# Performance work log

Hardware: AMD Instinct MI355X
Metric: run time of the kernel (lower is better)

## Reference

```python
import jax, jax.numpy as jnp
import numpy as np

B, L, C = 64, 4096, 16
PL, PC, NP, D, FS = 128, 8, 64, 64, 100  # patch_size_L, patch_size_C, num_patches, output_dim, f_s


def setup_inputs() -> dict:
    key = jax.random.key(0)
    ks = jax.random.split(key, 9)
    x = jax.random.normal(ks[0], (B, L, C), dtype=jnp.float32)
    start_L = jax.random.randint(ks[1], (B, NP), 0, L - PL + 1, dtype=jnp.int32)
    idx_C = jax.random.randint(ks[2], (B, NP, PC), 0, C, dtype=jnp.int32)
    W1 = jax.random.normal(ks[3], (2 * PC + 1, D), dtype=jnp.float32) * 0.2
    b1 = jax.random.normal(ks[4], (D,), dtype=jnp.float32) * 0.02
    W2 = jax.random.normal(ks[5], (2 * D + 1, D), dtype=jnp.float32) * 0.1
    b2 = jax.random.normal(ks[6], (D,), dtype=jnp.float32) * 0.02
    W3 = jax.random.normal(ks[7], (PL * D, D), dtype=jnp.float32) * 0.01
    b3 = jax.random.normal(ks[8], (D,), dtype=jnp.float32) * 0.02
    return dict(x=x, start_L=start_L, idx_C=idx_C, W1=W1, b1=b1, W2=W2, b2=b2, W3=W3, b3=b3)


def reference(x, start_L, idx_C, W1, b1, W2, b2, W3, b3):
    T = 1.0 / FS
    # contiguous window indices along L (wrapped), [B, NP, PL]
    idx_L = (start_L[:, :, None] + jnp.arange(PL, dtype=jnp.int32)) % L
    # fused double gather: avoid materializing the [B, NP, L, C] broadcast of the original
    bidx = jnp.arange(B)[:, None, None, None]
    patches = x[bidx, idx_L[:, :, :, None], idx_C[:, :, None, :]]        # [B, NP, PL, PC]
    # time embedding: t = arange(L)*T gathered by idx_L
    t_patches = (idx_L.astype(jnp.float32) * T)[..., None]               # [B, NP, PL, 1]
    # channel embedding: c = arange(C) gathered by idx_C
    c_patches = jnp.broadcast_to(idx_C.astype(jnp.float32)[:, :, None, :], (B, NP, PL, PC))
    feats = jnp.concatenate([patches, t_patches, c_patches], axis=-1)    # [B, NP, PL, 2*PC+1]
    h = jax.nn.silu(feats @ W1 + b1)                                     # [B, NP, PL, D]
    # --- fft branch (computed then discarded by the original module; kept for fidelity) ---
    f = jnp.linspace(0.0, FS / 2.0, PL // 2 + 1)
    fft = jnp.fft.rfft(h, axis=-2, norm='ortho')                         # [B, NP, PL//2+1, D]
    f_patches = jnp.broadcast_to(f[None, None, :, None], (B, NP, PL // 2 + 1, 1))
    fcat = jnp.concatenate([fft.real, fft.imag, f_patches], axis=-1)     # [B, NP, PL//2+1, 2D+1]
    _unused = jax.nn.silu(fcat @ W2 + b2)
    # --- mixer on flattened patches ---
    flat = h.reshape(B, NP, PL * D)                                      # [B, NP, PL*D]
    out = jax.nn.silu(flat @ W3 + b3)                                    # [B, NP, D]
    return out
```

## Files before the change

### kernel.cpp

```cpp
#include <hip/hip_runtime.h>
#include <hip/hip_bf16.h>

#define BB 64
#define LL 4096
#define CC 16
#define PL 128
#define PC 8
#define NPP 64
#define DD 64
#define TSTEP 0.01f

#define KSPLIT 4
#define LT_PER (PL / KSPLIT)
#define NT_MAIN 256
#define NMB BB

#define FRAG_U32 (PL * 8 * 256)
#define SPLIT_STRIDE (NMB * 2 * 2 * 64 * 16)
#define PART_FLT (KSPLIT * SPLIT_STRIDE)

typedef float f32x4  __attribute__((ext_vector_type(4)));
typedef float f32x16 __attribute__((ext_vector_type(16)));
typedef int   i32x4  __attribute__((ext_vector_type(4)));
typedef short s16x8  __attribute__((ext_vector_type(8)));
typedef unsigned int u32;

__device__ __forceinline__ float silu_f(float z) {
    return z * __builtin_amdgcn_rcpf(1.0f + __expf(-z));
}
__device__ __forceinline__ u32 pk(float lo, float hi) {
    __hip_bfloat162 p = __float22bfloat162_rn(float2{lo, hi});
    u32 r;
    __builtin_memcpy(&r, &p, 4);
    return r;
}
__device__ __forceinline__ s16x8 as8(i32x4 v) {
    s16x8 r;
    __builtin_memcpy(&r, &v, 16);
    return r;
}
__device__ __forceinline__ void plswap(u32& a, u32& b) {
    auto r = __builtin_amdgcn_permlane32_swap(a, b, false, false);
    u32 tmp[2];
    __builtin_memcpy(tmp, &r, 8);
    a = tmp[0]; b = tmp[1];
}

__global__ __launch_bounds__(256) void w3_prep(const float* __restrict__ W3,
                                               u32* __restrict__ wsf) {
    const int tid  = blockIdx.x * 256 + threadIdx.x;
    const int lane = tid & 63;
    const int m    = tid >> 6;
    const int ns   = m & 1;
    const int ksub = (m >> 1) & 1;
    const int kk   = (m >> 2) & 1;
    const int ltg  = m >> 3;
    const int k0   = ltg * 64 + kk * 32 + ksub * 16 + ((lane >> 5) << 3);
    const int col  = (ns << 5) + (lane & 31);
    u32 q[4];
    #pragma unroll
    for (int jj = 0; jj < 4; ++jj)
        q[jj] = pk(W3[(size_t)(k0 + 2 * jj)     * DD + col],
                   W3[(size_t)(k0 + 2 * jj + 1) * DD + col]);
    i32x4 v; v.x = (int)q[0]; v.y = (int)q[1]; v.z = (int)q[2]; v.w = (int)q[3];
    *(i32x4*)(wsf + (size_t)m * 256 + (lane << 2)) = v;
}

__global__ __launch_bounds__(NT_MAIN) void htfe_main(
    const float* __restrict__ x, const int* __restrict__ start_L,
    const int* __restrict__ idx_C, const float* __restrict__ W1,
    const float* __restrict__ b1, const u32* __restrict__ wsf,
    float* __restrict__ part)
{
    __shared__ __align__(64) float arena[512 * 17];
    __shared__ __align__(16) u32   xq[LT_PER * 256];
    __shared__ __align__(16) u32   cq[256];
    __shared__ int sStart[64];

    const int t    = threadIdx.x;
    const int lane = t & 63;
    const int w    = t >> 6;
    const int kk   = w >> 1;
    const int ph   = w & 1;
    const int l31  = lane & 31;
    const bool loH = lane < 32;

    const int mb    = blockIdx.x & (NMB - 1);
    const int split = blockIdx.x >> 6;
    const int b     = mb;
    const int lt0   = split * LT_PER;

    if (t < 64) sStart[t] = start_L[b * NPP + t];
    const int pGat = t & 63;
    const i32x4 ciA = *(const i32x4*)(idx_C + (size_t)b * NPP * PC + pGat * 8);
    const i32x4 ciB = *(const i32x4*)(idx_C + (size_t)b * NPP * PC + pGat * 8 + 4);
    if (t < 64) {
        cq[t * 4 + 0] = pk((float)ciA.x, (float)ciA.y);
        cq[t * 4 + 1] = pk((float)ciA.z, (float)ciA.w);
        cq[t * 4 + 2] = pk((float)ciB.x, (float)ciB.y);
        cq[t * 4 + 3] = pk((float)ciB.z, (float)ciB.w);
    }
    __syncthreads();

    #pragma unroll
    for (int pass = 0; pass < 4; ++pass) {
        #pragma unroll
        for (int q = 0; q < 8; ++q) {
            const int i    = q * 256 + t;
            const int row  = i >> 2;
            const int quad = i & 3;
            const int pp   = row & 63;
            const int gRow = sStart[pp] + lt0 + pass * 8 + (row >> 6);
            const f32x4 v = *(const f32x4*)(x + ((size_t)b * LL + (size_t)gRow) * CC + quad * 4);
            *(f32x4*)(arena + row * 17 + quad * 4) = v;
        }
        __syncthreads();
        #pragma unroll
        for (int g = 0; g < 2; ++g) {
            const int rr = g * 256 + t;
            const float* rb = arena + rr * 17;
            int cis[8];
            cis[0]=ciA.x; cis[1]=ciA.y; cis[2]=ciA.z; cis[3]=ciA.w;
            cis[4]=ciB.x; cis[5]=ciB.y; cis[6]=ciB.z; cis[7]=ciB.w;
            u32 qh[4];
            #pragma unroll
            for (int c2 = 0; c2 < 4; ++c2)
                qh[c2] = pk(rb[cis[2 * c2]], rb[cis[2 * c2 + 1]]);
            u32* dst = xq + (pass * 8 + (rr >> 6)) * 256 + (rr & 63) * 4;
            i32x4 vh; vh.x=(int)qh[0]; vh.y=(int)qh[1]; vh.z=(int)qh[2]; vh.w=(int)qh[3];
            *(i32x4*)dst = vh;
        }
        __syncthreads();
    }

    const int p  = ph * 32 + l31;
    const int dA = kk * 32 + l31;
    const float startPf = (float)sStart[p];

    i32x4 a1f0;
    if (loH) {
        a1f0.x = (int)pk(W1[0 * DD + dA], W1[1 * DD + dA]);
        a1f0.y = (int)pk(W1[2 * DD + dA], W1[3 * DD + dA]);
        a1f0.z = (int)pk(W1[4 * DD + dA], W1[5 * DD + dA]);
        a1f0.w = (int)pk(W1[6 * DD + dA], W1[7 * DD + dA]);
    } else {
        a1f0.x = (int)pk(W1[ 9 * DD + dA], W1[10 * DD + dA]);
        a1f0.y = (int)pk(W1[11 * DD + dA], W1[12 * DD + dA]);
        a1f0.z = (int)pk(W1[13 * DD + dA], W1[14 * DD + dA]);
        a1f0.w = (int)pk(W1[15 * DD + dA], W1[16 * DD + dA]);
    }
    f32x16 cb16, wt16;
    #pragma unroll
    for (int r = 0; r < 16; ++r) {
        const int dr = kk * 32 + (r & 3) + 8 * (r >> 2) + 4 * (lane >> 5);
        wt16[r] = W1[8 * DD + dr];
        cb16[r] = b1[dr];
    }

    f32x16 acc0 = {}, acc1 = {};
    const u32* bsrc = wsf + ((size_t)lt0 * 8 + (size_t)kk * 4) * 256 + (lane << 2);
    const u32* xrd     = loH ? (xq + p * 4) : (cq + p * 4);
    const int  xstride = loH ? 256 : 0;

    #pragma unroll 2
    for (int lt = 0; lt < LT_PER; ++lt) {
        const i32x4 bf00 = *(const i32x4*)(bsrc);
        const i32x4 bf01 = *(const i32x4*)(bsrc + 256);
        const i32x4 bf10 = *(const i32x4*)(bsrc + 512);
        const i32x4 bf11 = *(const i32x4*)(bsrc + 768);
        bsrc += 2048;

        const i32x4 rd = *(const i32x4*)xrd;
        xrd += xstride;

        const float tf = (startPf + (float)(lt0 + lt)) * TSTEP;
        f32x16 hp;
        #pragma unroll
        for (int r = 0; r < 16; ++r) hp[r] = cb16[r] + tf * wt16[r];
        hp = __builtin_amdgcn_mfma_f32_32x32x16_bf16(as8(a1f0), as8(rd), hp, 0, 0, 0);

        u32 P[8];
        #pragma unroll
        for (int j = 0; j < 8; ++j)
            P[j] = pk(silu_f(hp[2 * j]), silu_f(hp[2 * j + 1]));

        plswap(P[0], P[2]); plswap(P[1], P[3]);
        plswap(P[4], P[6]); plswap(P[5], P[7]);
        i32x4 af0; af0.x=(int)P[0]; af0.y=(int)P[1]; af0.z=(int)P[2]; af0.w=(int)P[3];
        i32x4 af1; af1.x=(int)P[4]; af1.y=(int)P[5]; af1.z=(int)P[6]; af1.w=(int)P[7];

        acc0 = __builtin_amdgcn_mfma_f32_32x32x16_bf16(as8(af0), as8(bf00), acc0, 0, 0, 0);
        acc0 = __builtin_amdgcn_mfma_f32_32x32x16_bf16(as8(af1), as8(bf10), acc0, 0, 0, 0);
        acc1 = __builtin_amdgcn_mfma_f32_32x32x16_bf16(as8(af0), as8(bf01), acc1, 0, 0, 0);
        acc1 = __builtin_amdgcn_mfma_f32_32x32x16_bf16(as8(af1), as8(bf11), acc1, 0, 0, 0);
    }

    f32x16* redacc = (f32x16*)arena;
    __syncthreads();
    if (kk == 1) {
        redacc[(ph * 2 + 0) * 64 + lane] = acc0;
        redacc[(ph * 2 + 1) * 64 + lane] = acc1;
    }
    __syncthreads();
    if (kk == 0) {
        const f32x16 r0 = redacc[(ph * 2 + 0) * 64 + lane];
        const f32x16 r1 = redacc[(ph * 2 + 1) * 64 + lane];
        float* pd0 = part + ((((size_t)split * NMB + mb) * 2 + ph) * 2 + 0) * 1024 + (lane << 4);
        float* pd1 = pd0 + 1024;
        #pragma unroll
        for (int q = 0; q < 4; ++q) {
            f32x4 o0, o1;
            #pragma unroll
            for (int j = 0; j < 4; ++j) {
                o0[j] = acc0[q * 4 + j] + r0[q * 4 + j];
                o1[j] = acc1[q * 4 + j] + r1[q * 4 + j];
            }
            *(f32x4*)(pd0 + q * 4) = o0;
            *(f32x4*)(pd1 + q * 4) = o1;
        }
    }
}

__global__ __launch_bounds__(256) void finish_reduce(const float* __restrict__ part,
                                                     const float* __restrict__ b3,
                                                     float* __restrict__ out) {
    const int bid   = blockIdx.x;
    const int mb    = bid & 63;
    const int chunk = bid >> 6;
    const int idx10 = chunk * 256 + threadIdx.x;
    const int rq   = idx10 & 3;
    const int lane = (idx10 >> 2) & 63;
    const int ns   = (idx10 >> 8) & 1;
    const int ph   = (idx10 >> 9) & 1;
    const int l31  = lane & 31;
    const float* src = part + (((size_t)mb * 2 + ph) * 2 + ns) * 1024 + (lane << 4) + (rq << 2);
    f32x4 s = {0.f, 0.f, 0.f, 0.f};
    #pragma unroll
    for (int sp = 0; sp < KSPLIT; ++sp) {
        const f32x4 v = *(const f32x4*)(src + (size_t)sp * SPLIT_STRIDE);
        s.x += v.x; s.y += v.y; s.z += v.z; s.w += v.w;
    }
    const int col  = (ns << 5) + l31;
    const float bias = b3[col];
    #pragma unroll
    for (int j = 0; j < 4; ++j) {
        const int prow = ph * 32 + j + 8 * rq + 4 * (lane >> 5);
        out[(size_t)(mb * NPP + prow) * DD + col] = silu_f(s[j] + bias);
    }
}

extern "C" void kernel_launch(void* const* d_in, const int* in_sizes, int n_in,
                              void* d_out, int out_size, void* d_ws, size_t ws_size,
                              hipStream_t stream) {
    const float* x       = (const float*)d_in[0];
    const int*   start_L = (const int*)  d_in[1];
    const int*   idx_C   = (const int*)  d_in[2];
    const float* W1      = (const float*)d_in[3];
    const float* b1      = (const float*)d_in[4];
    const float* W3      = (const float*)d_in[7];
    const float* b3      = (const float*)d_in[8];
    float* out  = (float*)d_out;
    u32*   wsf  = (u32*)d_ws;
    float* part = (float*)(wsf + FRAG_U32);

    w3_prep<<<256, 256, 0, stream>>>(W3, wsf);
    htfe_main<<<NMB * KSPLIT, NT_MAIN, 0, stream>>>(x, start_L, idx_C, W1, b1, wsf, part);
    finish_reduce<<<256, 256, 0, stream>>>(part, b3, out);
}
```

Before: 32.19 us.

## Overlap x-row gather with MFMA compute via register-prefetched chunks

The up-front four-pass staging of gathered x rows into LDS becomes a chunked software pipeline. Each chunk's global loads are prefetched into registers while the previous chunk's MFMA loop runs, then written to LDS and gathered into bf16 fragments between chunks. This hides global-load latency behind tensor-core work instead of paying for all passes before compute starts. The cost is 32 extra VGPRs held across the compute loop, which may reduce occupancy, and the synchronisation points now sit inside the main loop.

```diff
diff --git a/kernel.cpp b/kernel.cpp
--- a/kernel.cpp
+++ b/kernel.cpp
@@ -12,6 +12,7 @@
 
 #define KSPLIT 4
 #define LT_PER (PL / KSPLIT)
+#define NCHUNK 4
 #define NT_MAIN 256
 #define NMB BB
 
@@ -102,19 +103,31 @@
     }
     __syncthreads();
 
-    #pragma unroll
-    for (int pass = 0; pass < 4; ++pass) {
+    f32x4 rv[8];
+    const int rowi  = t >> 2;
+    const int quadi = t & 3;
+
+    auto LOADROWS = [&](int c) {
         #pragma unroll
         for (int q = 0; q < 8; ++q) {
             const int i    = q * 256 + t;
             const int row  = i >> 2;
             const int quad = i & 3;
             const int pp   = row & 63;
-            const int gRow = sStart[pp] + lt0 + pass * 8 + (row >> 6);
-            const f32x4 v = *(const f32x4*)(x + ((size_t)b * LL + (size_t)gRow) * CC + quad * 4);
-            *(f32x4*)(arena + row * 17 + quad * 4) = v;
-        }
-        __syncthreads();
+            const int gRow = sStart[pp] + lt0 + c * 8 + (row >> 6);
+            rv[q] = *(const f32x4*)(x + ((size_t)b * LL + (size_t)gRow) * CC + quad * 4);
+        }
+    };
+    auto WRITEROWS = [&]() {
+        #pragma unroll
+        for (int q = 0; q < 8; ++q) {
+            const int i    = q * 256 + t;
+            const int row  = i >> 2;
+            const int quad = i & 3;
+            *(f32x4*)(arena + row * 17 + quad * 4) = rv[q];
+        }
+    };
+    auto GATHER = [&](int c) {
         #pragma unroll
         for (int g = 0; g < 2; ++g) {
             const int rr = g * 256 + t;
@@ -126,12 +139,19 @@
             #pragma unroll
             for (int c2 = 0; c2 < 4; ++c2)
                 qh[c2] = pk(rb[cis[2 * c2]], rb[cis[2 * c2 + 1]]);
-            u32* dst = xq + (pass * 8 + (rr >> 6)) * 256 + (rr & 63) * 4;
+            u32* dst = xq + (c * 8 + (rr >> 6)) * 256 + (rr & 63) * 4;
             i32x4 vh; vh.x=(int)qh[0]; vh.y=(int)qh[1]; vh.z=(int)qh[2]; vh.w=(int)qh[3];
             *(i32x4*)dst = vh;
         }
-        __syncthreads();
-    }
+    };
+    (void)rowi; (void)quadi;
+
+    LOADROWS(0);
+    WRITEROWS();
+    __syncthreads();
+    GATHER(0);
+    LOADROWS(1);
+    __syncthreads();
 
     const int p  = ph * 32 + l31;
     const int dA = kk * 32 + l31;
@@ -162,37 +182,46 @@
     const u32* xrd     = loH ? (xq + p * 4) : (cq + p * 4);
     const int  xstride = loH ? 256 : 0;
 
-    #pragma unroll 2
-    for (int lt = 0; lt < LT_PER; ++lt) {
-        const i32x4 bf00 = *(const i32x4*)(bsrc);
-        const i32x4 bf01 = *(const i32x4*)(bsrc + 256);
-        const i32x4 bf10 = *(const i32x4*)(bsrc + 512);
-        const i32x4 bf11 = *(const i32x4*)(bsrc + 768);
-        bsrc += 2048;
-
-        const i32x4 rd = *(const i32x4*)xrd;
-        xrd += xstride;
-
-        const float tf = (startPf + (float)(lt0 + lt)) * TSTEP;
-        f32x16 hp;
-        #pragma unroll
-        for (int r = 0; r < 16; ++r) hp[r] = cb16[r] + tf * wt16[r];
-        hp = __builtin_amdgcn_mfma_f32_32x32x16_bf16(as8(a1f0), as8(rd), hp, 0, 0, 0);
-
-        u32 P[8];
-        #pragma unroll
-        for (int j = 0; j < 8; ++j)
-            P[j] = pk(silu_f(hp[2 * j]), silu_f(hp[2 * j + 1]));
-
-        plswap(P[0], P[2]); plswap(P[1], P[3]);
-        plswap(P[4], P[6]); plswap(P[5], P[7]);
-        i32x4 af0; af0.x=(int)P[0]; af0.y=(int)P[1]; af0.z=(int)P[2]; af0.w=(int)P[3];
-        i32x4 af1; af1.x=(int)P[4]; af1.y=(int)P[5]; af1.z=(int)P[6]; af1.w=(int)P[7];
-
-        acc0 = __builtin_amdgcn_mfma_f32_32x32x16_bf16(as8(af0), as8(bf00), acc0, 0, 0, 0);
-        acc0 = __builtin_amdgcn_mfma_f32_32x32x16_bf16(as8(af1), as8(bf10), acc0, 0, 0, 0);
-        acc1 = __builtin_amdgcn_mfma_f32_32x32x16_bf16(as8(af0), as8(bf01), acc1, 0, 0, 0);
-        acc1 = __builtin_amdgcn_mfma_f32_32x32x16_bf16(as8(af1), as8(bf11), acc1, 0, 0, 0);
+    for (int c = 0; c < NCHUNK; ++c) {
+        #pragma unroll 2
+        for (int l8 = 0; l8 < 8; ++l8) {
+            const int lt = c * 8 + l8;
+            const i32x4 bf00 = *(const i32x4*)(bsrc);
+            const i32x4 bf01 = *(const i32x4*)(bsrc + 256);
+            const i32x4 bf10 = *(const i32x4*)(bsrc + 512);
+            const i32x4 bf11 = *(const i32x4*)(bsrc + 768);
+            bsrc += 2048;
+
+            const i32x4 rd = *(const i32x4*)(xrd + (size_t)lt * xstride);
+
+            const float tf = (startPf + (float)(lt0 + lt)) * TSTEP;
+            f32x16 hp;
+            #pragma unroll
+            for (int r = 0; r < 16; ++r) hp[r] = cb16[r] + tf * wt16[r];
+            hp = __builtin_amdgcn_mfma_f32_32x32x16_bf16(as8(a1f0), as8(rd), hp, 0, 0, 0);
+
+            u32 P[8];
+            #pragma unroll
+            for (int j = 0; j < 8; ++j)
+                P[j] = pk(silu_f(hp[2 * j]), silu_f(hp[2 * j + 1]));
+
+            plswap(P[0], P[2]); plswap(P[1], P[3]);
+            plswap(P[4], P[6]); plswap(P[5], P[7]);
+            i32x4 af0; af0.x=(int)P[0]; af0.y=(int)P[1]; af0.z=(int)P[2]; af0.w=(int)P[3];
+            i32x4 af1; af1.x=(int)P[4]; af1.y=(int)P[5]; af1.z=(int)P[6]; af1.w=(int)P[7];
+
+            acc0 = __builtin_amdgcn_mfma_f32_32x32x16_bf16(as8(af0), as8(bf00), acc0, 0, 0, 0);
+            acc0 = __builtin_amdgcn_mfma_f32_32x32x16_bf16(as8(af1), as8(bf10), acc0, 0, 0, 0);
+            acc1 = __builtin_amdgcn_mfma_f32_32x32x16_bf16(as8(af0), as8(bf01), acc1, 0, 0, 0);
+            acc1 = __builtin_amdgcn_mfma_f32_32x32x16_bf16(as8(af1), as8(bf11), acc1, 0, 0, 0);
+        }
+        if (c < NCHUNK - 1) {
+            WRITEROWS();
+            __syncthreads();
+            GATHER(c + 1);
+            if (c < NCHUNK - 2) LOADROWS(c + 2);
+            __syncthreads();
+        }
     }
 
     f32x16* redacc = (f32x16*)arena;
```

After: 33.36 us. 3.6% more time.
